# Performance work log

Measured on AMD Instinct MI355X. Metric: run time of the kernel, lower is better.

## Reference

```python
import jax, jax.numpy as jnp
import numpy as np

B, P, ENC, DEC, ATT = 256, 196, 2048, 512, 512


def setup_inputs() -> dict:
    key = jax.random.key(0)
    ks = jax.random.split(key, 8)
    s_enc = 1.0 / np.sqrt(ENC)
    s_dec = 1.0 / np.sqrt(DEC)
    s_att = 1.0 / np.sqrt(ATT)
    return {
        "encoder_out": jax.random.normal(ks[0], (B, P, ENC), jnp.float32),
        "decoder_hidden": jax.random.normal(ks[1], (B, DEC), jnp.float32),
        "W_enc": jax.random.uniform(ks[2], (ENC, ATT), jnp.float32, -s_enc, s_enc),
        "b_enc": jax.random.uniform(ks[3], (ATT,), jnp.float32, -s_enc, s_enc),
        "W_dec": jax.random.uniform(ks[4], (DEC, ATT), jnp.float32, -s_dec, s_dec),
        "b_dec": jax.random.uniform(ks[5], (ATT,), jnp.float32, -s_dec, s_dec),
        "W_full": jax.random.uniform(ks[6], (ATT,), jnp.float32, -s_att, s_att),
        "b_full": jax.random.uniform(ks[7], (), jnp.float32, -s_att, s_att),
    }


def reference(encoder_out, decoder_hidden, W_enc, b_enc, W_dec, b_dec, W_full, b_full):
    # att1: [B, P, ATT]; att2: [B, ATT]
    att1 = jnp.einsum("bpe,ea->bpa", encoder_out, W_enc) + b_enc
    att2 = decoder_hidden @ W_dec + b_dec
    # additive combine + relu + scalar projection -> [B, P]
    att = jnp.einsum("bpa,a->bp", jax.nn.relu(att1 + att2[:, None, :]), W_full) + b_full
    alpha = jax.nn.softmax(att, axis=1)  # softmax over pixels
    context_vector = jnp.einsum("bpe,bp->be", encoder_out, alpha)
    return (context_vector, alpha)
```

## Files before the change

### kernel.cpp

```cpp
#include <hip/hip_runtime.h>
#include <hip/hip_bf16.h>
#include <stdint.h>


using u16x8 = __attribute__((ext_vector_type(8))) unsigned short;
using s16x8 = __attribute__((ext_vector_type(8))) short;
using f32x4 = __attribute__((ext_vector_type(4))) float;

static __device__ __forceinline__ unsigned short f2b(float f) {
  unsigned int u = __builtin_bit_cast(unsigned int, f);
  u = u + 0x7fffu + ((u >> 16) & 1u);
  return (unsigned short)(u >> 16);
}

__global__ __launch_bounds__(256) void transpose_wenc(
    const float* __restrict__ wenc, unsigned short* __restrict__ wencT) {
  __shared__ unsigned short tile[32][34];
  const int t = threadIdx.x;
  const int x = t & 31, y = t >> 5;
  const int kb = blockIdx.x & 63, nb = blockIdx.x >> 6;
  const int k0 = kb << 5, n0 = nb << 5;
#pragma unroll
  for (int i = 0; i < 4; ++i) {
    int kk = y * 4 + i;
    tile[x][kk] = f2b(wenc[(size_t)(k0 + kk) * 512 + n0 + x]);
  }
  __syncthreads();
#pragma unroll
  for (int i = 0; i < 4; ++i) {
    int nn = y * 4 + i;
    wencT[(size_t)(n0 + nn) * 2048 + k0 + x] = tile[nn][x];
  }
}

__global__ __launch_bounds__(256) void comb_kernel(
    const float* __restrict__ dec, const float* __restrict__ wdec,
    const float* __restrict__ bdec, const float* __restrict__ benc,
    float* __restrict__ comb) {
  __shared__ float dec_sh[8][512];
  const int t = threadIdx.x;
  const int b0 = blockIdx.x * 8;
  for (int i = t; i < 8 * 512; i += 256)
    dec_sh[i >> 9][i & 511] = dec[(size_t)b0 * 512 + i];
  __syncthreads();
  const int a0 = 2 * t;
  float bias0 = bdec[a0] + benc[a0];
  float bias1 = bdec[a0 + 1] + benc[a0 + 1];
  float acc0[8], acc1[8];
#pragma unroll
  for (int i = 0; i < 8; ++i) { acc0[i] = bias0; acc1[i] = bias1; }
  for (int e = 0; e < 512; ++e) {
    float2 wv = *(const float2*)&wdec[(size_t)e * 512 + a0];
#pragma unroll
    for (int i = 0; i < 8; ++i) {
      float d = dec_sh[i][e];
      acc0[i] = fmaf(d, wv.x, acc0[i]);
      acc1[i] = fmaf(d, wv.y, acc1[i]);
    }
  }
#pragma unroll
  for (int i = 0; i < 8; ++i) {
    float2 o = make_float2(acc0[i], acc1[i]);
    *(float2*)&comb[(size_t)(b0 + i) * 512 + a0] = o;
  }
}

#define LROW 40

__global__ __launch_bounds__(512, 4) void gemm_att(
    const float* __restrict__ enc, const unsigned short* __restrict__ wencT,
    const float* __restrict__ comb, const float* __restrict__ wfull_g,
    float* __restrict__ att) {
  __shared__ alignas(16) unsigned short Ash[64 * LROW];
  __shared__ alignas(16) unsigned short Bsh[512 * LROW];
  __shared__ float comb_sh[1024];
  __shared__ float wfull_sh[512];
  __shared__ float att_sh[64];

  const int t = threadIdx.x;
  const int l = t & 63;
  const int w = t >> 6;
  const int quad = l >> 4, col = l & 15;
  const int wm = w >> 2, wn = w & 3;
  const int r0 = blockIdx.x * 64;
  const int b0 = r0 / 196;
  const int rsw = (b0 + 1) * 196;
  const int b1 = (b0 + 1 < 256) ? b0 + 1 : 255;

  comb_sh[t] = comb[(size_t)b0 * 512 + t];
  comb_sh[512 + t] = comb[(size_t)b1 * 512 + t];
  wfull_sh[t] = wfull_g[t];
  if (t < 64) att_sh[t] = 0.0f;

  const float* agp = enc + (size_t)(r0 + ((t & 255) >> 2)) * 2048 + (t & 3) * 8;
  unsigned short* alp = &Ash[((t & 255) >> 2) * LROW + (t & 3) * 8];
  const unsigned short* bgp[4];
  unsigned short* blp[4];
#pragma unroll
  for (int j = 0; j < 4; ++j) {
    int c = j * 512 + t;
    int n = c >> 2, kc = c & 3;
    bgp[j] = wencT + (size_t)n * 2048 + kc * 8;
    blp[j] = &Bsh[n * LROW + kc * 8];
  }

  int aoff[2], boff[8];
#pragma unroll
  for (int mt = 0; mt < 2; ++mt) {
    int ml = wm * 32 + mt * 16 + col;
    aoff[mt] = ml * LROW + quad * 8;
  }
#pragma unroll
  for (int nt = 0; nt < 8; ++nt) {
    int nl = wn * 128 + nt * 16 + col;
    boff[nt] = nl * LROW + quad * 8;
  }

  f32x4 acc[2][8];
#pragma unroll
  for (int mt = 0; mt < 2; ++mt)
#pragma unroll
    for (int nt = 0; nt < 8; ++nt) acc[mt][nt] = (f32x4){0.f, 0.f, 0.f, 0.f};

  for (int ks = 0; ks < 64; ++ks) {
    f32x4 a0v, a1v;
    if (t < 256) {
      a0v = *(const f32x4*)agp;
      a1v = *(const f32x4*)(agp + 4);
    }
    u16x8 bv[4];
#pragma unroll
    for (int j = 0; j < 4; ++j) bv[j] = *(const u16x8*)bgp[j];

    __syncthreads();
    if (t < 256) {
      u16x8 av;
      av[0] = f2b(a0v[0]); av[1] = f2b(a0v[1]);
      av[2] = f2b(a0v[2]); av[3] = f2b(a0v[3]);
      av[4] = f2b(a1v[0]); av[5] = f2b(a1v[1]);
      av[6] = f2b(a1v[2]); av[7] = f2b(a1v[3]);
      *(u16x8*)alp = av;
    }
#pragma unroll
    for (int j = 0; j < 4; ++j) *(u16x8*)blp[j] = bv[j];
    __syncthreads();

    s16x8 afr[2];
#pragma unroll
    for (int mt = 0; mt < 2; ++mt) afr[mt] = *(const s16x8*)&Ash[aoff[mt]];
#pragma unroll
    for (int nt = 0; nt < 8; ++nt) {
      s16x8 bfr = *(const s16x8*)&Bsh[boff[nt]];
      acc[0][nt] = __builtin_amdgcn_mfma_f32_16x16x32_bf16(afr[0], bfr, acc[0][nt], 0, 0, 0);
      acc[1][nt] = __builtin_amdgcn_mfma_f32_16x16x32_bf16(afr[1], bfr, acc[1][nt], 0, 0, 0);
    }

    agp += 32;
#pragma unroll
    for (int j = 0; j < 4; ++j) bgp[j] += 32;
  }

  __syncthreads();
#pragma unroll
  for (int mt = 0; mt < 2; ++mt) {
#pragma unroll
    for (int r = 0; r < 4; ++r) {
      int rl = wm * 32 + mt * 16 + quad * 4 + r;
      int cb = ((r0 + rl) >= rsw) ? 512 : 0;
      float s = 0.f;
#pragma unroll
      for (int nt = 0; nt < 8; ++nt) {
        int n = wn * 128 + nt * 16 + col;
        float v = acc[mt][nt][r] + comb_sh[cb + n];
        v = fmaxf(v, 0.f);
        s = fmaf(v, wfull_sh[n], s);
      }
      s += __shfl_xor(s, 1);
      s += __shfl_xor(s, 2);
      s += __shfl_xor(s, 4);
      s += __shfl_xor(s, 8);
      if (col == 0) atomicAdd(&att_sh[rl], s);
    }
  }
  __syncthreads();
  if (t < 64) att[(size_t)r0 + t] = att_sh[t];
}

__global__ __launch_bounds__(256) void softmax_ctx(
    const float* __restrict__ att, const float* __restrict__ enc,
    float* __restrict__ ctx_out, float* __restrict__ alpha_out) {
  const int b = blockIdx.x, t = threadIdx.x;
  __shared__ float red[256];
  __shared__ float alpha_sh[196];

  float v = (t < 196) ? att[(size_t)b * 196 + t] : -1e30f;
  red[t] = v;
  __syncthreads();
  for (int s = 128; s > 0; s >>= 1) {
    if (t < s) red[t] = fmaxf(red[t], red[t + s]);
    __syncthreads();
  }
  float mx = red[0];
  __syncthreads();
  float e = (t < 196) ? __expf(v - mx) : 0.f;
  red[t] = e;
  __syncthreads();
  for (int s = 128; s > 0; s >>= 1) {
    if (t < s) red[t] += red[t + s];
    __syncthreads();
  }
  float a = e / red[0];
  if (t < 196) {
    alpha_sh[t] = a;
    alpha_out[(size_t)b * 196 + t] = a;
  }
  __syncthreads();

  float acc[8] = {0.f, 0.f, 0.f, 0.f, 0.f, 0.f, 0.f, 0.f};
  const float* ep = enc + (size_t)b * 196 * 2048 + t * 8;
#pragma unroll 2
  for (int p = 0; p < 196; ++p) {
    float ap = alpha_sh[p];
    f32x4 e0 = *(const f32x4*)(ep);
    f32x4 e1 = *(const f32x4*)(ep + 4);
    acc[0] = fmaf(ap, e0[0], acc[0]);
    acc[1] = fmaf(ap, e0[1], acc[1]);
    acc[2] = fmaf(ap, e0[2], acc[2]);
    acc[3] = fmaf(ap, e0[3], acc[3]);
    acc[4] = fmaf(ap, e1[0], acc[4]);
    acc[5] = fmaf(ap, e1[1], acc[5]);
    acc[6] = fmaf(ap, e1[2], acc[6]);
    acc[7] = fmaf(ap, e1[3], acc[7]);
    ep += 2048;
  }
  float* op = ctx_out + (size_t)b * 2048 + t * 8;
  *(f32x4*)op = (f32x4){acc[0], acc[1], acc[2], acc[3]};
  *(f32x4*)(op + 4) = (f32x4){acc[4], acc[5], acc[6], acc[7]};
}

extern "C" void kernel_launch(void* const* d_in, const int* in_sizes, int n_in,
                              void* d_out, int out_size, void* d_ws, size_t ws_size,
                              hipStream_t stream) {
  (void)in_sizes; (void)n_in; (void)out_size; (void)ws_size;
  const float* enc   = (const float*)d_in[0];
  const float* dec   = (const float*)d_in[1];
  const float* wenc  = (const float*)d_in[2];
  const float* benc  = (const float*)d_in[3];
  const float* wdec  = (const float*)d_in[4];
  const float* bdec  = (const float*)d_in[5];
  const float* wfull = (const float*)d_in[6];

  unsigned short* wencT = (unsigned short*)d_ws;
  float* comb = (float*)((char*)d_ws + (2u << 20));
  float* att  = (float*)((char*)d_ws + (2u << 20) + (512u << 10));

  float* ctx_out = (float*)d_out;
  float* alpha_out = ctx_out + (size_t)256 * 2048;

  hipLaunchKernelGGL(transpose_wenc, dim3(1024), dim3(256), 0, stream, wenc, wencT);
  hipLaunchKernelGGL(comb_kernel, dim3(32), dim3(256), 0, stream, dec, wdec, bdec, benc, comb);
  hipLaunchKernelGGL(gemm_att, dim3(784), dim3(512), 0, stream, enc, wencT, comb, wfull, att);
  hipLaunchKernelGGL(softmax_ctx, dim3(256), dim3(256), 0, stream, att, enc, ctx_out, alpha_out);
}
```

Measured before the change: 830.5 us.

## Double-buffer GEMM with direct global-to-LDS loads, swizzled layout, more parallel aux kernels

```diff
diff --git a/kernel.cpp b/kernel.cpp
--- a/kernel.cpp
+++ b/kernel.cpp
@@ -1,11 +1,13 @@
 #include <hip/hip_runtime.h>
-#include <hip/hip_bf16.h>
 #include <stdint.h>
 
 
 using u16x8 = __attribute__((ext_vector_type(8))) unsigned short;
 using s16x8 = __attribute__((ext_vector_type(8))) short;
 using f32x4 = __attribute__((ext_vector_type(4))) float;
+
+typedef __attribute__((address_space(1))) const void gvoid_t;
+typedef __attribute__((address_space(3))) void lvoid_t;
 
 static __device__ __forceinline__ unsigned short f2b(float f) {
   unsigned int u = __builtin_bit_cast(unsigned int, f);
@@ -13,74 +15,61 @@
   return (unsigned short)(u >> 16);
 }
 
+static __device__ __forceinline__ void glds16(const void* g, void* l) {
+  __builtin_amdgcn_global_load_lds((gvoid_t*)g, (lvoid_t*)l, 16, 0, 0);
+}
+
 __global__ __launch_bounds__(256) void transpose_wenc(
     const float* __restrict__ wenc, unsigned short* __restrict__ wencT) {
-  __shared__ unsigned short tile[32][34];
-  const int t = threadIdx.x;
-  const int x = t & 31, y = t >> 5;
-  const int kb = blockIdx.x & 63, nb = blockIdx.x >> 6;
-  const int k0 = kb << 5, n0 = nb << 5;
-#pragma unroll
-  for (int i = 0; i < 4; ++i) {
-    int kk = y * 4 + i;
-    tile[x][kk] = f2b(wenc[(size_t)(k0 + kk) * 512 + n0 + x]);
-  }
-  __syncthreads();
-#pragma unroll
-  for (int i = 0; i < 4; ++i) {
-    int nn = y * 4 + i;
-    wencT[(size_t)(n0 + nn) * 2048 + k0 + x] = tile[nn][x];
-  }
+  const int g = blockIdx.x * 256 + threadIdx.x;
+  const int ks = g >> 11;
+  const int c = g & 2047;
+  const int n = c >> 2;
+  const int kc = c & 3;
+  const float* src = wenc + (size_t)(ks * 32 + kc * 8) * 512 + n;
+  u16x8 v;
+#pragma unroll
+  for (int j = 0; j < 8; ++j) v[j] = f2b(src[(size_t)j * 512]);
+  const int idx = (n * 32 + kc * 8) ^ ((n & 7) << 3);
+  *(u16x8*)&wencT[(size_t)ks * 16384 + idx] = v;
 }
 
 __global__ __launch_bounds__(256) void comb_kernel(
     const float* __restrict__ dec, const float* __restrict__ wdec,
     const float* __restrict__ bdec, const float* __restrict__ benc,
     float* __restrict__ comb) {
-  __shared__ float dec_sh[8][512];
-  const int t = threadIdx.x;
-  const int b0 = blockIdx.x * 8;
-  for (int i = t; i < 8 * 512; i += 256)
-    dec_sh[i >> 9][i & 511] = dec[(size_t)b0 * 512 + i];
+  __shared__ float dec_sh[512];
+  const int b = blockIdx.x, t = threadIdx.x;
+  dec_sh[t] = dec[(size_t)b * 512 + t];
+  dec_sh[256 + t] = dec[(size_t)b * 512 + 256 + t];
   __syncthreads();
   const int a0 = 2 * t;
-  float bias0 = bdec[a0] + benc[a0];
-  float bias1 = bdec[a0 + 1] + benc[a0 + 1];
-  float acc0[8], acc1[8];
-#pragma unroll
-  for (int i = 0; i < 8; ++i) { acc0[i] = bias0; acc1[i] = bias1; }
+  float acc0 = bdec[a0] + benc[a0];
+  float acc1 = bdec[a0 + 1] + benc[a0 + 1];
+#pragma unroll 8
   for (int e = 0; e < 512; ++e) {
     float2 wv = *(const float2*)&wdec[(size_t)e * 512 + a0];
-#pragma unroll
-    for (int i = 0; i < 8; ++i) {
-      float d = dec_sh[i][e];
-      acc0[i] = fmaf(d, wv.x, acc0[i]);
-      acc1[i] = fmaf(d, wv.y, acc1[i]);
-    }
-  }
-#pragma unroll
-  for (int i = 0; i < 8; ++i) {
-    float2 o = make_float2(acc0[i], acc1[i]);
-    *(float2*)&comb[(size_t)(b0 + i) * 512 + a0] = o;
-  }
-}
-
-#define LROW 40
+    float d = dec_sh[e];
+    acc0 = fmaf(d, wv.x, acc0);
+    acc1 = fmaf(d, wv.y, acc1);
+  }
+  *(float2*)&comb[(size_t)b * 512 + a0] = make_float2(acc0, acc1);
+}
 
 __global__ __launch_bounds__(512, 4) void gemm_att(
     const float* __restrict__ enc, const unsigned short* __restrict__ wencT,
     const float* __restrict__ comb, const float* __restrict__ wfull_g,
     float* __restrict__ att) {
-  __shared__ alignas(16) unsigned short Ash[64 * LROW];
-  __shared__ alignas(16) unsigned short Bsh[512 * LROW];
+  __shared__ alignas(16) unsigned short Bsh[2][16384];
+  __shared__ alignas(16) unsigned short Ash[2][2048];
   __shared__ float comb_sh[1024];
   __shared__ float wfull_sh[512];
   __shared__ float att_sh[64];
 
   const int t = threadIdx.x;
   const int l = t & 63;
+  const int quad = l >> 4, col = l & 15;
   const int w = t >> 6;
-  const int quad = l >> 4, col = l & 15;
   const int wm = w >> 2, wn = w & 3;
   const int r0 = blockIdx.x * 64;
   const int b0 = r0 / 196;
@@ -92,28 +81,29 @@
   wfull_sh[t] = wfull_g[t];
   if (t < 64) att_sh[t] = 0.0f;
 
-  const float* agp = enc + (size_t)(r0 + ((t & 255) >> 2)) * 2048 + (t & 3) * 8;
-  unsigned short* alp = &Ash[((t & 255) >> 2) * LROW + (t & 3) * 8];
+  const int arow = (t & 255) >> 2, achk = t & 3;
+  const float* ap = enc + (size_t)(r0 + arow) * 2048 + achk * 8;
+  const int a_lds = (arow * 32 + achk * 8) ^ ((arow & 7) << 3);
+
   const unsigned short* bgp[4];
-  unsigned short* blp[4];
+  int blds[4];
 #pragma unroll
   for (int j = 0; j < 4; ++j) {
-    int c = j * 512 + t;
-    int n = c >> 2, kc = c & 3;
-    bgp[j] = wencT + (size_t)n * 2048 + kc * 8;
-    blp[j] = &Bsh[n * LROW + kc * 8];
+    const int c = j * 512 + t;
+    bgp[j] = wencT + (size_t)c * 8;
+    blds[j] = c * 8;
   }
 
   int aoff[2], boff[8];
 #pragma unroll
   for (int mt = 0; mt < 2; ++mt) {
-    int ml = wm * 32 + mt * 16 + col;
-    aoff[mt] = ml * LROW + quad * 8;
+    const int row = wm * 32 + mt * 16 + col;
+    aoff[mt] = (row * 32 + quad * 8) ^ ((row & 7) << 3);
   }
 #pragma unroll
   for (int nt = 0; nt < 8; ++nt) {
-    int nl = wn * 128 + nt * 16 + col;
-    boff[nt] = nl * LROW + quad * 8;
+    const int n = wn * 128 + nt * 16 + col;
+    boff[nt] = (n * 32 + quad * 8) ^ ((n & 7) << 3);
   }
 
   f32x4 acc[2][8];
@@ -122,42 +112,63 @@
 #pragma unroll
     for (int nt = 0; nt < 8; ++nt) acc[mt][nt] = (f32x4){0.f, 0.f, 0.f, 0.f};
 
+#pragma unroll
+  for (int j = 0; j < 4; ++j) {
+    glds16(bgp[j], &Bsh[0][blds[j]]);
+    bgp[j] += 16384;
+  }
+  if (t < 256) {
+    f32x4 a0v = *(const f32x4*)ap;
+    f32x4 a1v = *(const f32x4*)(ap + 4);
+    u16x8 av;
+    av[0] = f2b(a0v[0]); av[1] = f2b(a0v[1]); av[2] = f2b(a0v[2]); av[3] = f2b(a0v[3]);
+    av[4] = f2b(a1v[0]); av[5] = f2b(a1v[1]); av[6] = f2b(a1v[2]); av[7] = f2b(a1v[3]);
+    *(u16x8*)&Ash[0][a_lds] = av;
+  }
+  ap += 32;
+  __syncthreads();
+
+#pragma unroll 2
   for (int ks = 0; ks < 64; ++ks) {
+    const int buf = ks & 1, nbuf = buf ^ 1;
+    const bool pf = (ks < 63);
+
     f32x4 a0v, a1v;
-    if (t < 256) {
-      a0v = *(const f32x4*)agp;
-      a1v = *(const f32x4*)(agp + 4);
-    }
-    u16x8 bv[4];
-#pragma unroll
-    for (int j = 0; j < 4; ++j) bv[j] = *(const u16x8*)bgp[j];
-
-    __syncthreads();
-    if (t < 256) {
+    if (pf && t < 256) {
+      a0v = *(const f32x4*)ap;
+      a1v = *(const f32x4*)(ap + 4);
+    }
+    __builtin_amdgcn_sched_barrier(0);
+    if (pf) {
+#pragma unroll
+      for (int j = 0; j < 4; ++j) {
+        glds16(bgp[j], &Bsh[nbuf][blds[j]]);
+        bgp[j] += 16384;
+      }
+    }
+    __builtin_amdgcn_sched_barrier(0);
+
+    s16x8 afr0 = *(const s16x8*)&Ash[buf][aoff[0]];
+    s16x8 afr1 = *(const s16x8*)&Ash[buf][aoff[1]];
+#pragma unroll
+    for (int nt = 0; nt < 8; ++nt) {
+      s16x8 bfr = *(const s16x8*)&Bsh[buf][boff[nt]];
+      acc[0][nt] = __builtin_amdgcn_mfma_f32_16x16x32_bf16(afr0, bfr, acc[0][nt], 0, 0, 0);
+      acc[1][nt] = __builtin_amdgcn_mfma_f32_16x16x32_bf16(afr1, bfr, acc[1][nt], 0, 0, 0);
+    }
+    __builtin_amdgcn_sched_barrier(0);
+
+    if (pf && t < 256) {
       u16x8 av;
-      av[0] = f2b(a0v[0]); av[1] = f2b(a0v[1]);
-      av[2] = f2b(a0v[2]); av[3] = f2b(a0v[3]);
-      av[4] = f2b(a1v[0]); av[5] = f2b(a1v[1]);
-      av[6] = f2b(a1v[2]); av[7] = f2b(a1v[3]);
-      *(u16x8*)alp = av;
-    }
-#pragma unroll
-    for (int j = 0; j < 4; ++j) *(u16x8*)blp[j] = bv[j];
-    __syncthreads();
-
-    s16x8 afr[2];
-#pragma unroll
-    for (int mt = 0; mt < 2; ++mt) afr[mt] = *(const s16x8*)&Ash[aoff[mt]];
-#pragma unroll
-    for (int nt = 0; nt < 8; ++nt) {
-      s16x8 bfr = *(const s16x8*)&Bsh[boff[nt]];
-      acc[0][nt] = __builtin_amdgcn_mfma_f32_16x16x32_bf16(afr[0], bfr, acc[0][nt], 0, 0, 0);
-      acc[1][nt] = __builtin_amdgcn_mfma_f32_16x16x32_bf16(afr[1], bfr, acc[1][nt], 0, 0, 0);
-    }
-
-    agp += 32;
-#pragma unroll
-    for (int j = 0; j < 4; ++j) bgp[j] += 32;
+      av[0] = f2b(a0v[0]); av[1] = f2b(a0v[1]); av[2] = f2b(a0v[2]); av[3] = f2b(a0v[3]);
+      av[4] = f2b(a1v[0]); av[5] = f2b(a1v[1]); av[6] = f2b(a1v[2]); av[7] = f2b(a1v[3]);
+      *(u16x8*)&Ash[nbuf][a_lds] = av;
+      ap += 32;
+    }
+    __builtin_amdgcn_sched_barrier(0);
+    asm volatile("s_waitcnt vmcnt(0) lgkmcnt(0)" ::: "memory");
+    __builtin_amdgcn_sched_barrier(0);
+    __builtin_amdgcn_s_barrier();
   }
 
   __syncthreads();
@@ -165,12 +176,12 @@
   for (int mt = 0; mt < 2; ++mt) {
 #pragma unroll
     for (int r = 0; r < 4; ++r) {
-      int rl = wm * 32 + mt * 16 + quad * 4 + r;
-      int cb = ((r0 + rl) >= rsw) ? 512 : 0;
+      const int rl = wm * 32 + mt * 16 + quad * 4 + r;
+      const int cb = ((r0 + rl) >= rsw) ? 512 : 0;
       float s = 0.f;
 #pragma unroll
       for (int nt = 0; nt < 8; ++nt) {
-        int n = wn * 128 + nt * 16 + col;
+        const int n = wn * 128 + nt * 16 + col;
         float v = acc[mt][nt][r] + comb_sh[cb + n];
         v = fmaxf(v, 0.f);
         s = fmaf(v, wfull_sh[n], s);
@@ -189,7 +200,8 @@
 __global__ __launch_bounds__(256) void softmax_ctx(
     const float* __restrict__ att, const float* __restrict__ enc,
     float* __restrict__ ctx_out, float* __restrict__ alpha_out) {
-  const int b = blockIdx.x, t = threadIdx.x;
+  const int b = blockIdx.x >> 1, slice = blockIdx.x & 1;
+  const int t = threadIdx.x;
   __shared__ float red[256];
   __shared__ float alpha_sh[196];
 
@@ -212,30 +224,23 @@
   float a = e / red[0];
   if (t < 196) {
     alpha_sh[t] = a;
-    alpha_out[(size_t)b * 196 + t] = a;
-  }
-  __syncthreads();
-
-  float acc[8] = {0.f, 0.f, 0.f, 0.f, 0.f, 0.f, 0.f, 0.f};
-  const float* ep = enc + (size_t)b * 196 * 2048 + t * 8;
-#pragma unroll 2
+    if (slice == 0) alpha_out[(size_t)b * 196 + t] = a;
+  }
+  __syncthreads();
+
+  f32x4 acc = {0.f, 0.f, 0.f, 0.f};
+  const float* ep = enc + (size_t)b * 196 * 2048 + slice * 1024 + t * 4;
+#pragma unroll 4
   for (int p = 0; p < 196; ++p) {
     float ap = alpha_sh[p];
-    f32x4 e0 = *(const f32x4*)(ep);
-    f32x4 e1 = *(const f32x4*)(ep + 4);
-    acc[0] = fmaf(ap, e0[0], acc[0]);
-    acc[1] = fmaf(ap, e0[1], acc[1]);
-    acc[2] = fmaf(ap, e0[2], acc[2]);
-    acc[3] = fmaf(ap, e0[3], acc[3]);
-    acc[4] = fmaf(ap, e1[0], acc[4]);
-    acc[5] = fmaf(ap, e1[1], acc[5]);
-    acc[6] = fmaf(ap, e1[2], acc[6]);
-    acc[7] = fmaf(ap, e1[3], acc[7]);
+    f32x4 ev = *(const f32x4*)ep;
+    acc[0] = fmaf(ap, ev[0], acc[0]);
+    acc[1] = fmaf(ap, ev[1], acc[1]);
+    acc[2] = fmaf(ap, ev[2], acc[2]);
+    acc[3] = fmaf(ap, ev[3], acc[3]);
     ep += 2048;
   }
-  float* op = ctx_out + (size_t)b * 2048 + t * 8;
-  *(f32x4*)op = (f32x4){acc[0], acc[1], acc[2], acc[3]};
-  *(f32x4*)(op + 4) = (f32x4){acc[4], acc[5], acc[6], acc[7]};
+  *(f32x4*)(ctx_out + (size_t)b * 2048 + slice * 1024 + t * 4) = acc;
 }
 
 extern "C" void kernel_launch(void* const* d_in, const int* in_sizes, int n_in,
@@ -257,8 +262,8 @@
   float* ctx_out = (float*)d_out;
   float* alpha_out = ctx_out + (size_t)256 * 2048;
 
-  hipLaunchKernelGGL(transpose_wenc, dim3(1024), dim3(256), 0, stream, wenc, wencT);
-  hipLaunchKernelGGL(comb_kernel, dim3(32), dim3(256), 0, stream, dec, wdec, bdec, benc, comb);
+  hipLaunchKernelGGL(transpose_wenc, dim3(512), dim3(256), 0, stream, wenc, wencT);
+  hipLaunchKernelGGL(comb_kernel, dim3(256), dim3(256), 0, stream, dec, wdec, bdec, benc, comb);
   hipLaunchKernelGGL(gemm_att, dim3(784), dim3(512), 0, stream, enc, wencT, comb, wfull, att);
-  hipLaunchKernelGGL(softmax_ctx, dim3(256), dim3(256), 0, stream, att, enc, ctx_out, alpha_out);
-}
+  hipLaunchKernelGGL(softmax_ctx, dim3(512), dim3(256), 0, stream, att, enc, ctx_out, alpha_out);
+}
```

After: 734.7 us. 11.5% less time.
